# Performance work log

Measured on AMD Instinct MI355X. Metric: run time of the kernel, lower is better.

The kernel has to match this reference:

```python
import jax, jax.numpy as jnp
import numpy as np

B, T, V, D, H, C = 64, 512, 50000, 128, 256, 50


def setup_inputs() -> dict:
    key = jax.random.key(0)
    ks = jax.random.split(key, 15)
    s = 0.05
    rn = lambda k, shape: jax.random.normal(k, shape, jnp.float32) * s
    words = jax.random.randint(ks[0], (B, T), 0, V)
    target = jax.random.randint(ks[1], (B, T), 0, C)
    seq_len = jax.random.randint(ks[2], (B,), T // 2, T + 1)
    seq_len = seq_len.at[0].set(T)  # ensure at least one full-length sequence
    return dict(
        words=words, target=target, seq_len=seq_len,
        emb=rn(ks[3], (V, D)),
        W_ih_f=rn(ks[4], (4 * H, D)), W_hh_f=rn(ks[5], (4 * H, H)), b_f=rn(ks[6], (4 * H,)),
        W_ih_b=rn(ks[7], (4 * H, D)), W_hh_b=rn(ks[8], (4 * H, H)), b_b=rn(ks[9], (4 * H,)),
        fc_W=rn(ks[10], (C, 2 * H)), fc_b=rn(ks[11], (C,)),
        trans=rn(ks[12], (C, C)), start_s=rn(ks[13], (C,)), end_s=rn(ks[14], (C,)),
    )


def _lstm(x, W_ih, W_hh, b):
    # unidirectional LSTM, PyTorch gate order (i, f, g, o). x: [B,T,D] -> h: [B,T,H]
    Hh = W_hh.shape[1]
    xg = jnp.einsum('btd,gd->btg', x, W_ih) + b  # [B,T,4H]

    def step(carry, xt):
        h, c = carry
        g = xt + h @ W_hh.T
        i, f, gg, o = jnp.split(g, 4, axis=-1)
        c = jax.nn.sigmoid(f) * c + jax.nn.sigmoid(i) * jnp.tanh(gg)
        h = jax.nn.sigmoid(o) * jnp.tanh(c)
        return (h, c), h

    h0 = jnp.zeros((x.shape[0], Hh), x.dtype)
    _, hs = jax.lax.scan(step, (h0, h0), jnp.swapaxes(xg, 0, 1))
    return jnp.swapaxes(hs, 0, 1)


def _rev_idx(seq_len, t_len):
    # per-sequence time-reversal indices (packed-sequence semantics for the backward LSTM)
    t = jnp.arange(t_len)[None, :]
    L = seq_len[:, None]
    return jnp.where(t < L, L - 1 - t, t)


def _bilstm_crf_loss(words, target, seq_len, emb, W_ih_f, W_hh_f, b_f,
                     W_ih_b, W_hh_b, b_b, fc_W, fc_b, trans, start_s, end_s):
    x = emb[words]  # [B,T,D]
    h_f = _lstm(x, W_ih_f, W_hh_f, b_f)
    idx = _rev_idx(seq_len, x.shape[1])
    x_rev = jnp.take_along_axis(x, idx[:, :, None], axis=1)
    h_b = jnp.take_along_axis(_lstm(x_rev, W_ih_b, W_hh_b, b_b), idx[:, :, None], axis=1)
    feats = jnp.concatenate([h_f, h_b], axis=-1) @ fc_W.T + fc_b  # [B,T,C]
    logits = jax.nn.log_softmax(feats, axis=-1)
    mask = jnp.arange(x.shape[1])[None, :] < seq_len[:, None]  # [B,T] bool

    # --- CRF normalizer (forward algorithm) ---
    alpha0 = logits[:, 0] + start_s  # [B,C]

    def step(alpha, inp):
        emit_t, m_t = inp  # [B,C], [B]
        tmp = alpha[:, :, None] + trans[None, :, :] + emit_t[:, None, :]
        new = jax.nn.logsumexp(tmp, axis=1)
        return jnp.where(m_t[:, None], new, alpha), None

    alpha, _ = jax.lax.scan(step, alpha0,
                            (jnp.swapaxes(logits, 0, 1)[1:], jnp.swapaxes(mask, 0, 1)[1:]))
    norm = jax.nn.logsumexp(alpha + end_s, axis=1)  # [B]

    # --- gold path score ---
    maskf = mask.astype(logits.dtype)
    emit = jnp.take_along_axis(logits, target[:, :, None], axis=2)[..., 0]  # [B,T]
    trans_sc = trans[target[:, :-1], target[:, 1:]]  # [B,T-1]
    last = target[jnp.arange(target.shape[0]), seq_len - 1]
    gold = (emit * maskf).sum(1) + (trans_sc * maskf[:, 1:]).sum(1) \
           + start_s[target[:, 0]] + end_s[last]

    return jnp.mean(norm - gold)


def reference(words, target, seq_len, emb, W_ih_f, W_hh_f, b_f,
              W_ih_b, W_hh_b, b_b, fc_W, fc_b, trans, start_s, end_s):
    return _bilstm_crf_loss(words, target, seq_len, emb, W_ih_f, W_hh_f, b_f,
                            W_ih_b, W_hh_b, b_b, fc_W, fc_b, trans, start_s, end_s)
```

## Files before the change

kernel.cpp:

```cpp
#include <hip/hip_runtime.h>
#include <hip/hip_bf16.h>

#define BB 64
#define TT 512
#define DD 128
#define HH 256
#define G4 1024
#define CC 50

typedef __bf16 bf16x8 __attribute__((ext_vector_type(8)));
typedef float  f32x4  __attribute__((ext_vector_type(4)));
typedef _Float16 h16x2 __attribute__((ext_vector_type(2)));

#if defined(__has_builtin)
#if __has_builtin(__builtin_amdgcn_fdot2)
#define HAS_FDOT2 1
#endif
#endif

__device__ __forceinline__ float bl16(unsigned u) { return __uint_as_float(u << 16); }
__device__ __forceinline__ float bh16(unsigned u) { return __uint_as_float(u & 0xffff0000u); }

__device__ __forceinline__ float sigf(float x) {
    return 1.f / (1.f + __expf(-x));
}
__device__ __forceinline__ float tanh_s(float x) {
    float ax = fabsf(x);
    float e = __expf(-2.f * ax);
    float r = (1.f - e) / (1.f + e);
    return copysignf(r, x);
}

__device__ __forceinline__ float dot8(float acc, uint4 w, uint4 h) {
#ifdef HAS_FDOT2
    acc = __builtin_amdgcn_fdot2(__builtin_bit_cast(h16x2, w.x),
                                 __builtin_bit_cast(h16x2, h.x), acc, false);
    acc = __builtin_amdgcn_fdot2(__builtin_bit_cast(h16x2, w.y),
                                 __builtin_bit_cast(h16x2, h.y), acc, false);
    acc = __builtin_amdgcn_fdot2(__builtin_bit_cast(h16x2, w.z),
                                 __builtin_bit_cast(h16x2, h.z), acc, false);
    acc = __builtin_amdgcn_fdot2(__builtin_bit_cast(h16x2, w.w),
                                 __builtin_bit_cast(h16x2, h.w), acc, false);
#else
    {
        h16x2 a = __builtin_bit_cast(h16x2, w.x), b = __builtin_bit_cast(h16x2, h.x);
        acc = fmaf((float)a.x, (float)b.x, acc); acc = fmaf((float)a.y, (float)b.y, acc);
        a = __builtin_bit_cast(h16x2, w.y); b = __builtin_bit_cast(h16x2, h.y);
        acc = fmaf((float)a.x, (float)b.x, acc); acc = fmaf((float)a.y, (float)b.y, acc);
        a = __builtin_bit_cast(h16x2, w.z); b = __builtin_bit_cast(h16x2, h.z);
        acc = fmaf((float)a.x, (float)b.x, acc); acc = fmaf((float)a.y, (float)b.y, acc);
        a = __builtin_bit_cast(h16x2, w.w); b = __builtin_bit_cast(h16x2, h.w);
        acc = fmaf((float)a.x, (float)b.x, acc); acc = fmaf((float)a.y, (float)b.y, acc);
    }
#endif
    return acc;
}

__global__ __launch_bounds__(256) void k_cvt(
    const float* __restrict__ src, __hip_bfloat16* __restrict__ dst, int n)
{
    int i = (blockIdx.x * 256 + threadIdx.x) * 8;
    if (i + 8 <= n) {
        float4 a = *(const float4*)(src + i);
        float4 b = *(const float4*)(src + i + 4);
        __hip_bfloat16 o[8];
        o[0] = __float2bfloat16(a.x); o[1] = __float2bfloat16(a.y);
        o[2] = __float2bfloat16(a.z); o[3] = __float2bfloat16(a.w);
        o[4] = __float2bfloat16(b.x); o[5] = __float2bfloat16(b.y);
        o[6] = __float2bfloat16(b.z); o[7] = __float2bfloat16(b.w);
        *(uint4*)(dst + i) = *(const uint4*)o;
    }
}

__global__ __launch_bounds__(256) void k_pack(
    const float* __restrict__ Wf, const float* __restrict__ Wb,
    uint4* __restrict__ Wp)
{
    int blk = blockIdx.x;
    int g   = blk & 3;
    int kc  = (blk >> 2) & 31;
    int dir = blk >> 7;
    int j = threadIdx.x;
    int row = g * 256 + j;
    const float* src = (dir ? Wb : Wf) + (size_t)row * 256 + kc * 8;
    float4 a = *(const float4*)src;
    float4 b = *(const float4*)(src + 4);
    _Float16 o[8];
    o[0] = (_Float16)a.x; o[1] = (_Float16)a.y;
    o[2] = (_Float16)a.z; o[3] = (_Float16)a.w;
    o[4] = (_Float16)b.x; o[5] = (_Float16)b.y;
    o[6] = (_Float16)b.z; o[7] = (_Float16)b.w;
    Wp[((size_t)(dir * 32 + kc) * 4 + g) * 256 + j] = *(const uint4*)o;
}

__global__ __launch_bounds__(256, 2) void k_xg(
    const int* __restrict__ words,
    const float* __restrict__ embf,
    const __hip_bfloat16* __restrict__ Wih,
    const float* __restrict__ bfv, const float* __restrict__ bbv,
    __hip_bfloat16* __restrict__ xg)
{
    __shared__ __align__(16) __hip_bfloat16 A[64][136];
    int tid = threadIdx.x;
    int bt0 = blockIdx.x * 64;

    {
        int r = tid >> 2;
        int c0 = (tid & 3) * 32;
        int word = words[bt0 + r];
        const float* src = embf + (size_t)word * DD + c0;
#pragma unroll
        for (int i = 0; i < 8; ++i) {
            float4 v = *(const float4*)(src + i * 4);
            __hip_bfloat16 o[4] = {__float2bfloat16(v.x), __float2bfloat16(v.y),
                                   __float2bfloat16(v.z), __float2bfloat16(v.w)};
            *(uint2*)&A[r][c0 + i * 4] = *(const uint2*)o;
        }
    }
    __syncthreads();

    int wave = tid >> 6, lane = tid & 63;
    int m = lane & 15, quad = lane >> 4;

    bf16x8 afr[4][4];
#pragma unroll
    for (int ms = 0; ms < 4; ++ms)
#pragma unroll
        for (int kf = 0; kf < 4; ++kf)
            afr[ms][kf] = *(const bf16x8*)&A[ms * 16 + m][quad * 8 + kf * 32];

#pragma unroll 1
    for (int i = 0; i < 32; ++i) {
        int nt = wave * 32 + i;
        int gate_g = nt * 16 + m;
        int dir = gate_g >> 10;
        int gate = gate_g & 1023;
        const __hip_bfloat16* brow = Wih + (size_t)gate_g * DD + quad * 8;
        bf16x8 bfr[4];
#pragma unroll
        for (int kf = 0; kf < 4; ++kf) bfr[kf] = *(const bf16x8*)(brow + kf * 32);
        float bv = dir ? bbv[gate] : bfv[gate];
        size_t dbase = (size_t)dir * (size_t)(BB * TT * G4);

#pragma unroll
        for (int ms = 0; ms < 4; ++ms) {
            f32x4 acc = {0.f, 0.f, 0.f, 0.f};
#pragma unroll
            for (int kf = 0; kf < 4; ++kf)
                acc = __builtin_amdgcn_mfma_f32_16x16x32_bf16(afr[ms][kf], bfr[kf], acc, 0, 0, 0);
#pragma unroll
            for (int r = 0; r < 4; ++r) {
                int btrow = bt0 + ms * 16 + quad * 4 + r;
                xg[dbase + (size_t)btrow * G4 + gate] = __float2bfloat16(acc[r] + bv);
            }
        }
    }
}

__global__ __launch_bounds__(512)
__attribute__((amdgpu_waves_per_eu(2, 2)))
void k_lstm(
    const __hip_bfloat16* __restrict__ xg,
    const uint4* __restrict__ Wp,
    const int* __restrict__ seq_len,
    __hip_bfloat16* __restrict__ hcat)
{
    int b = blockIdx.x & 63;
    int dir = blockIdx.x >> 6;
    int tid = threadIdx.x;
    int j   = tid & 255;
    int half = tid >> 8;

    __shared__ __align__(16) uint4 wlds[12 * 512];
    __shared__ __align__(16) _Float16 hbf[2][HH];
    __shared__ float pbuf[4][HH];

    const uint4* Wd = Wp + (size_t)dir * (32 * 4 * 256);

    uint4 wr[13][4];
#pragma unroll
    for (int kcl = 0; kcl < 13; ++kcl)
#pragma unroll
        for (int g = 0; g < 4; ++g)
            wr[kcl][g] = Wd[(((kcl + 16 * half) * 4 + g) * 256) + j];
#pragma unroll
    for (int kcl = 0; kcl < 13; ++kcl)
#pragma unroll
        for (int g = 0; g < 4; ++g)
            asm volatile("" : "+v"(wr[kcl][g].x), "+v"(wr[kcl][g].y),
                              "+v"(wr[kcl][g].z), "+v"(wr[kcl][g].w));

#pragma unroll
    for (int kcl = 13; kcl < 16; ++kcl)
#pragma unroll
        for (int g = 0; g < 4; ++g)
            wlds[((kcl - 13) * 4 + g) * 512 + tid] =
                Wd[(((kcl + 16 * half) * 4 + g) * 256) + j];

    if (half == 0) hbf[0][j] = (_Float16)0.f;
    float c = 0.f;
    int L = seq_len[b];
    const __hip_bfloat16* xgb = xg + (size_t)dir * (size_t)(BB * TT * G4)
                                   + (size_t)b * TT * G4;

    int tc = dir ? (L - 1) : 0;
    float xv0 = 0.f, xv1 = 0.f, xv2 = 0.f, xv3 = 0.f;
    if (half == 0) {
        const __hip_bfloat16* xr = xgb + (size_t)tc * G4 + j;
        xv0 = __bfloat162float(xr[0]);   xv1 = __bfloat162float(xr[256]);
        xv2 = __bfloat162float(xr[512]); xv3 = __bfloat162float(xr[768]);
    }
    __syncthreads();

    for (int t = 0; t < TT; ++t) {
        int cur = t & 1, nxt = cur ^ 1;
        int tn = t + 1;
        int tcn = dir ? ((tn < L) ? (L - 1 - tn) : tn) : tn;
        bool pf = (tn < TT);
        __hip_bfloat16 p0, p1, p2, p3;
        if (half == 0 && pf) {
            const __hip_bfloat16* xr = xgb + (size_t)tcn * G4 + j;
            p0 = xr[0]; p1 = xr[256]; p2 = xr[512]; p3 = xr[768];
        }

        unsigned off = 0;
        asm volatile("" : "+v"(off));

        const _Float16* hrow = &hbf[cur][half * 128];
        float a0 = 0.f, a1 = 0.f, a2 = 0.f, a3 = 0.f;
#pragma unroll
        for (int kcl = 0; kcl < 13; ++kcl) {
            uint4 hv = *(const uint4*)(hrow + kcl * 8);
            a0 = dot8(a0, wr[kcl][0], hv);
            a1 = dot8(a1, wr[kcl][1], hv);
            a2 = dot8(a2, wr[kcl][2], hv);
            a3 = dot8(a3, wr[kcl][3], hv);
        }
#pragma unroll
        for (int kcl = 13; kcl < 16; ++kcl) {
            uint4 hv = *(const uint4*)(hrow + kcl * 8);
            int m0 = (kcl - 13) * 4;
            a0 = dot8(a0, wlds[(m0 + 0) * 512 + tid + off], hv);
            a1 = dot8(a1, wlds[(m0 + 1) * 512 + tid + off], hv);
            a2 = dot8(a2, wlds[(m0 + 2) * 512 + tid + off], hv);
            a3 = dot8(a3, wlds[(m0 + 3) * 512 + tid + off], hv);
        }

        if (half) {
            pbuf[0][j] = a0; pbuf[1][j] = a1;
            pbuf[2][j] = a2; pbuf[3][j] = a3;
        }
        __syncthreads();

        if (half == 0) {
            float gi = a0 + pbuf[0][j] + xv0;
            float gf = a1 + pbuf[1][j] + xv1;
            float gg = a2 + pbuf[2][j] + xv2;
            float go = a3 + pbuf[3][j] + xv3;
            float i_ = sigf(gi), f_ = sigf(gf), G = tanh_s(gg), o_ = sigf(go);
            c = f_ * c + i_ * G;
            float h = o_ * tanh_s(c);
            hbf[nxt][j] = (_Float16)h;
            hcat[((size_t)(b * TT + tc)) * (2 * HH) + dir * HH + j] = __float2bfloat16(h);
            if (pf) {
                xv0 = __bfloat162float(p0); xv1 = __bfloat162float(p1);
                xv2 = __bfloat162float(p2); xv3 = __bfloat162float(p3);
            }
        }
        tc = tcn;
        __syncthreads();
    }
}

__global__ __launch_bounds__(64) void k_fc(
    const __hip_bfloat16* __restrict__ hcat,
    const __hip_bfloat16* __restrict__ fcW,
    const float* __restrict__ fcb,
    float* __restrict__ logits)
{
    int row = blockIdx.x;
    int tid = threadIdx.x;
    __shared__ __align__(16) float hrow[2 * HH];
    __shared__ float fbuf[CC + 2];

    {
        uint4 v = *(const uint4*)(hcat + (size_t)row * (2 * HH) + tid * 8);
        float* d = &hrow[tid * 8];
        d[0] = bl16(v.x); d[1] = bh16(v.x);
        d[2] = bl16(v.y); d[3] = bh16(v.y);
        d[4] = bl16(v.z); d[5] = bh16(v.z);
        d[6] = bl16(v.w); d[7] = bh16(v.w);
    }
    __syncthreads();

    if (tid < CC) {
        float acc = fcb[tid];
        const uint4* wr = (const uint4*)(fcW + (size_t)tid * (2 * HH));
#pragma unroll 8
        for (int kc = 0; kc < 64; ++kc) {
            uint4 wv = wr[kc];
            float4 h0 = *(const float4*)&hrow[kc * 8];
            float4 h1 = *(const float4*)&hrow[kc * 8 + 4];
            acc = fmaf(bl16(wv.x), h0.x, acc); acc = fmaf(bh16(wv.x), h0.y, acc);
            acc = fmaf(bl16(wv.y), h0.z, acc); acc = fmaf(bh16(wv.y), h0.w, acc);
            acc = fmaf(bl16(wv.z), h1.x, acc); acc = fmaf(bh16(wv.z), h1.y, acc);
            acc = fmaf(bl16(wv.w), h1.z, acc); acc = fmaf(bh16(wv.w), h1.w, acc);
        }
        fbuf[tid] = acc;
    }
    __syncthreads();

    float m = -1e30f;
    for (int i = 0; i < CC; ++i) m = fmaxf(m, fbuf[i]);
    float s = 0.f;
    for (int i = 0; i < CC; ++i) s += __expf(fbuf[i] - m);
    float lns = __logf(s);
    if (tid < CC) logits[(size_t)row * CC + tid] = fbuf[tid] - m - lns;
}

__global__ __launch_bounds__(256) void k_crf(
    const float* __restrict__ logits,
    const int* __restrict__ target,
    const int* __restrict__ seq_len,
    const float* __restrict__ trans,
    const float* __restrict__ start_s,
    const float* __restrict__ end_s,
    float* __restrict__ loss_b)
{
    const float L2E = 1.4426950408889634f;
    const float LN2 = 0.6931471805599453f;
    int b = blockIdx.x;
    int tid = threadIdx.x;
    int q = tid >> 6;
    int j = tid & 63;
    bool act = (j < CC);
    int L = seq_len[b];
    const float* lg = logits + (size_t)b * TT * CC;

    __shared__ float alpha2[64];
    __shared__ float mpart[4][64];
    __shared__ float spart[4][64];
    __shared__ float red[256];
    __shared__ float nbuf[CC + 2];

    int i0 = q * 13;
    int icnt = min(13, CC - i0);
    float treg[13];
    if (act) {
#pragma unroll
        for (int s = 0; s < 13; ++s)
            if (s < icnt) treg[s] = L2E * trans[(i0 + s) * CC + j];
    }
    if (q == 0 && act) alpha2[j] = L2E * (lg[j] + start_s[j]);
    __syncthreads();

    float v[13];
    for (int t = 1; t < L; ++t) {
        float mq = -1e30f;
        if (act) {
#pragma unroll
            for (int s = 0; s < 13; ++s)
                if (s < icnt) { v[s] = alpha2[i0 + s] + treg[s]; mq = fmaxf(mq, v[s]); }
        }
        mpart[q][j] = mq;
        __syncthreads();
        float M = fmaxf(fmaxf(mpart[0][j], mpart[1][j]), fmaxf(mpart[2][j], mpart[3][j]));
        float sq = 0.f;
        if (act) {
#pragma unroll
            for (int s = 0; s < 13; ++s)
                if (s < icnt) sq += exp2f(v[s] - M);
        }
        spart[q][j] = sq;
        __syncthreads();
        if (q == 0 && act) {
            float S = spart[0][j] + spart[1][j] + spart[2][j] + spart[3][j];
            alpha2[j] = M + log2f(S) + L2E * lg[(size_t)t * CC + j];
        }
        __syncthreads();
    }

    if (q == 0 && act) nbuf[j] = alpha2[j] + L2E * end_s[j];

    float gp = 0.f;
    const int* tg = target + b * TT;
    for (int t = tid; t < TT; t += 256) {
        if (t < L) {
            int c = tg[t];
            gp += lg[(size_t)t * CC + c];
            if (t >= 1) gp += trans[tg[t - 1] * CC + c];
        }
    }
    red[tid] = gp;
    __syncthreads();

    if (tid == 0) {
        float m2 = -1e30f;
        for (int i = 0; i < CC; ++i) m2 = fmaxf(m2, nbuf[i]);
        float s2 = 0.f;
        for (int i = 0; i < CC; ++i) s2 += exp2f(nbuf[i] - m2);
        float norm_nat = (m2 + log2f(s2)) * LN2;
        float g = 0.f;
        for (int i = 0; i < 256; ++i) g += red[i];
        g += start_s[tg[0]] + end_s[tg[L - 1]];
        loss_b[b] = norm_nat - g;
    }
}

__global__ void k_fin(const float* __restrict__ loss_b, float* __restrict__ out)
{
    int t = threadIdx.x;
    float v = loss_b[t];
#pragma unroll
    for (int o = 32; o > 0; o >>= 1) v += __shfl_down(v, o);
    if (t == 0) out[0] = v * (1.f / BB);
}

extern "C" void kernel_launch(void* const* d_in, const int* in_sizes, int n_in,
                              void* d_out, int out_size, void* d_ws, size_t ws_size,
                              hipStream_t stream)
{
    const int* words   = (const int*)d_in[0];
    const int* target  = (const int*)d_in[1];
    const int* seq_len = (const int*)d_in[2];
    const float* emb    = (const float*)d_in[3];
    const float* W_ih_f = (const float*)d_in[4];
    const float* W_hh_f = (const float*)d_in[5];
    const float* b_f    = (const float*)d_in[6];
    const float* W_ih_b = (const float*)d_in[7];
    const float* W_hh_b = (const float*)d_in[8];
    const float* b_b    = (const float*)d_in[9];
    const float* fc_W   = (const float*)d_in[10];
    const float* fc_b   = (const float*)d_in[11];
    const float* trans  = (const float*)d_in[12];
    const float* start_s= (const float*)d_in[13];
    const float* end_s  = (const float*)d_in[14];

    char* ws = (char*)d_ws;
    __hip_bfloat16* xg     = (__hip_bfloat16*)ws;
    __hip_bfloat16* hcat   = (__hip_bfloat16*)(ws + 134217728);
    float*          logits = (float*)(ws + 167772160);
    uint4*          Wp     = (uint4*)(ws + 167772160);
    float*          loss_b = (float*)(ws + 174325760);
    __hip_bfloat16* wihall = (__hip_bfloat16*)(ws + 174326016);
    __hip_bfloat16* fcw_bf = (__hip_bfloat16*)(ws + 174850304);

    k_cvt<<<64,  256, 0, stream>>>(W_ih_f, wihall,          131072);
    k_cvt<<<64,  256, 0, stream>>>(W_ih_b, wihall + 131072, 131072);
    k_cvt<<<13,  256, 0, stream>>>(fc_W,   fcw_bf,          25600);
    k_pack<<<256, 256, 0, stream>>>(W_hh_f, W_hh_b, Wp);

    k_xg  <<<512, 256, 0, stream>>>(words, emb, wihall, b_f, b_b, xg);
    k_lstm<<<128, 512, 0, stream>>>(xg, Wp, seq_len, hcat);
    k_fc  <<<32768, 64, 0, stream>>>(hcat, fcw_bf, fc_b, logits);
    k_crf <<<64, 256, 0, stream>>>(logits, target, seq_len, trans, start_s, end_s, loss_b);
    k_fin <<<1, 64, 0, stream>>>(loss_b, (float*)d_out);
}
```

Baseline: 1.809 ms.

## Stream LSTM recurrent weights from cache, batch FC rows, prefetch CRF emissions

The LSTM kernel stops keeping 13 of its 16 weight chunks in registers. It now keeps 4 in registers, 4 in an enlarged LDS buffer, and reloads the other 8 from global memory on every timestep in two staged batches. This frees registers, but adds per-step global or L2 traffic on the serial critical path. The FC kernel now handles four rows per 256-thread block to cut block count, and the CRF kernel prefetches the next timestep's emission value into a register.

```diff
diff --git a/kernel.cpp b/kernel.cpp
--- a/kernel.cpp
+++ b/kernel.cpp
@@ -157,8 +157,7 @@
     }
 }
 
-__global__ __launch_bounds__(512)
-__attribute__((amdgpu_waves_per_eu(2, 2)))
+__global__ __launch_bounds__(512, 2)
 void k_lstm(
     const __hip_bfloat16* __restrict__ xg,
     const uint4* __restrict__ Wp,
@@ -171,31 +170,25 @@
     int j   = tid & 255;
     int half = tid >> 8;
 
-    __shared__ __align__(16) uint4 wlds[12 * 512];
+    __shared__ __align__(16) uint4 wlds[16 * 512];
     __shared__ __align__(16) _Float16 hbf[2][HH];
     __shared__ float pbuf[4][HH];
 
     const uint4* Wd = Wp + (size_t)dir * (32 * 4 * 256);
-
-    uint4 wr[13][4];
-#pragma unroll
-    for (int kcl = 0; kcl < 13; ++kcl)
+    const uint4* Ws = Wd + (size_t)(16 * half) * 4 * 256 + j;
+
+    uint4 wh[4][4];
+#pragma unroll
+    for (int kcl = 0; kcl < 4; ++kcl)
 #pragma unroll
         for (int g = 0; g < 4; ++g)
-            wr[kcl][g] = Wd[(((kcl + 16 * half) * 4 + g) * 256) + j];
-#pragma unroll
-    for (int kcl = 0; kcl < 13; ++kcl)
+            wh[kcl][g] = Ws[(kcl * 4 + g) * 256];
+
+#pragma unroll
+    for (int kcl = 12; kcl < 16; ++kcl)
 #pragma unroll
         for (int g = 0; g < 4; ++g)
-            asm volatile("" : "+v"(wr[kcl][g].x), "+v"(wr[kcl][g].y),
-                              "+v"(wr[kcl][g].z), "+v"(wr[kcl][g].w));
-
-#pragma unroll
-    for (int kcl = 13; kcl < 16; ++kcl)
-#pragma unroll
-        for (int g = 0; g < 4; ++g)
-            wlds[((kcl - 13) * 4 + g) * 512 + tid] =
-                Wd[(((kcl + 16 * half) * 4 + g) * 256) + j];
+            wlds[((kcl - 12) * 4 + g) * 512 + tid] = Ws[(kcl * 4 + g) * 256];
 
     if (half == 0) hbf[0][j] = (_Float16)0.f;
     float c = 0.f;
@@ -212,7 +205,15 @@
     }
     __syncthreads();
 
+#pragma unroll 1
     for (int t = 0; t < TT; ++t) {
+#pragma unroll
+        for (int kcl = 0; kcl < 4; ++kcl)
+#pragma unroll
+            for (int g = 0; g < 4; ++g)
+                asm volatile("" : "+v"(wh[kcl][g].x), "+v"(wh[kcl][g].y),
+                                  "+v"(wh[kcl][g].z), "+v"(wh[kcl][g].w));
+
         int cur = t & 1, nxt = cur ^ 1;
         int tn = t + 1;
         int tcn = dir ? ((tn < L) ? (L - 1 - tn) : tn) : tn;
@@ -228,22 +229,55 @@
 
         const _Float16* hrow = &hbf[cur][half * 128];
         float a0 = 0.f, a1 = 0.f, a2 = 0.f, a3 = 0.f;
-#pragma unroll
-        for (int kcl = 0; kcl < 13; ++kcl) {
+
+        uint4 s1[4][4];
+#pragma unroll
+        for (int q = 0; q < 4; ++q)
+#pragma unroll
+            for (int g = 0; g < 4; ++g)
+                s1[q][g] = Ws[((q + 4) * 4 + g) * 256];
+
+#pragma unroll
+        for (int kcl = 0; kcl < 4; ++kcl) {
             uint4 hv = *(const uint4*)(hrow + kcl * 8);
-            a0 = dot8(a0, wr[kcl][0], hv);
-            a1 = dot8(a1, wr[kcl][1], hv);
-            a2 = dot8(a2, wr[kcl][2], hv);
-            a3 = dot8(a3, wr[kcl][3], hv);
-        }
-#pragma unroll
-        for (int kcl = 13; kcl < 16; ++kcl) {
+            a0 = dot8(a0, wh[kcl][0], hv);
+            a1 = dot8(a1, wh[kcl][1], hv);
+            a2 = dot8(a2, wh[kcl][2], hv);
+            a3 = dot8(a3, wh[kcl][3], hv);
+        }
+
+#pragma unroll
+        for (int kcl = 12; kcl < 16; ++kcl) {
             uint4 hv = *(const uint4*)(hrow + kcl * 8);
-            int m0 = (kcl - 13) * 4;
+            int m0 = (kcl - 12) * 4;
             a0 = dot8(a0, wlds[(m0 + 0) * 512 + tid + off], hv);
             a1 = dot8(a1, wlds[(m0 + 1) * 512 + tid + off], hv);
             a2 = dot8(a2, wlds[(m0 + 2) * 512 + tid + off], hv);
             a3 = dot8(a3, wlds[(m0 + 3) * 512 + tid + off], hv);
+        }
+
+        uint4 s2[4][4];
+#pragma unroll
+        for (int q = 0; q < 4; ++q)
+#pragma unroll
+            for (int g = 0; g < 4; ++g)
+                s2[q][g] = Ws[((q + 8) * 4 + g) * 256];
+
+#pragma unroll
+        for (int q = 0; q < 4; ++q) {
+            uint4 hv = *(const uint4*)(hrow + (q + 4) * 8);
+            a0 = dot8(a0, s1[q][0], hv);
+            a1 = dot8(a1, s1[q][1], hv);
+            a2 = dot8(a2, s1[q][2], hv);
+            a3 = dot8(a3, s1[q][3], hv);
+        }
+#pragma unroll
+        for (int q = 0; q < 4; ++q) {
+            uint4 hv = *(const uint4*)(hrow + (q + 8) * 8);
+            a0 = dot8(a0, s2[q][0], hv);
+            a1 = dot8(a1, s2[q][1], hv);
+            a2 = dot8(a2, s2[q][2], hv);
+            a3 = dot8(a3, s2[q][3], hv);
         }
 
         if (half) {
@@ -272,20 +306,21 @@
     }
 }
 
-__global__ __launch_bounds__(64) void k_fc(
+__global__ __launch_bounds__(256) void k_fc(
     const __hip_bfloat16* __restrict__ hcat,
     const __hip_bfloat16* __restrict__ fcW,
     const float* __restrict__ fcb,
     float* __restrict__ logits)
 {
-    int row = blockIdx.x;
-    int tid = threadIdx.x;
-    __shared__ __align__(16) float hrow[2 * HH];
-    __shared__ float fbuf[CC + 2];
+    int team = threadIdx.x >> 6;
+    int tid  = threadIdx.x & 63;
+    int row  = blockIdx.x * 4 + team;
+    __shared__ __align__(16) float hrow[4][2 * HH];
+    __shared__ float fbuf[4][CC + 2];
 
     {
         uint4 v = *(const uint4*)(hcat + (size_t)row * (2 * HH) + tid * 8);
-        float* d = &hrow[tid * 8];
+        float* d = &hrow[team][tid * 8];
         d[0] = bl16(v.x); d[1] = bh16(v.x);
         d[2] = bl16(v.y); d[3] = bh16(v.y);
         d[4] = bl16(v.z); d[5] = bh16(v.z);
@@ -299,23 +334,23 @@
 #pragma unroll 8
         for (int kc = 0; kc < 64; ++kc) {
             uint4 wv = wr[kc];
-            float4 h0 = *(const float4*)&hrow[kc * 8];
-            float4 h1 = *(const float4*)&hrow[kc * 8 + 4];
+            float4 h0 = *(const float4*)&hrow[team][kc * 8];
+            float4 h1 = *(const float4*)&hrow[team][kc * 8 + 4];
             acc = fmaf(bl16(wv.x), h0.x, acc); acc = fmaf(bh16(wv.x), h0.y, acc);
             acc = fmaf(bl16(wv.y), h0.z, acc); acc = fmaf(bh16(wv.y), h0.w, acc);
             acc = fmaf(bl16(wv.z), h1.x, acc); acc = fmaf(bh16(wv.z), h1.y, acc);
             acc = fmaf(bl16(wv.w), h1.z, acc); acc = fmaf(bh16(wv.w), h1.w, acc);
         }
-        fbuf[tid] = acc;
+        fbuf[team][tid] = acc;
     }
     __syncthreads();
 
     float m = -1e30f;
-    for (int i = 0; i < CC; ++i) m = fmaxf(m, fbuf[i]);
+    for (int i = 0; i < CC; ++i) m = fmaxf(m, fbuf[team][i]);
     float s = 0.f;
-    for (int i = 0; i < CC; ++i) s += __expf(fbuf[i] - m);
+    for (int i = 0; i < CC; ++i) s += __expf(fbuf[team][i] - m);
     float lns = __logf(s);
-    if (tid < CC) logits[(size_t)row * CC + tid] = fbuf[tid] - m - lns;
+    if (tid < CC) logits[(size_t)row * CC + tid] = fbuf[team][tid] - m - lns;
 }
 
 __global__ __launch_bounds__(256) void k_crf(
@@ -355,7 +390,13 @@
     __syncthreads();
 
     float v[13];
+    float lgreg = 0.f;
+    if (q == 0 && act) lgreg = lg[CC + j];
     for (int t = 1; t < L; ++t) {
+        float lgnext = 0.f;
+        if (q == 0 && act && (t + 1) < L)
+            lgnext = lg[(size_t)(t + 1) * CC + j];
+
         float mq = -1e30f;
         if (act) {
 #pragma unroll
@@ -375,8 +416,9 @@
         __syncthreads();
         if (q == 0 && act) {
             float S = spart[0][j] + spart[1][j] + spart[2][j] + spart[3][j];
-            alpha2[j] = M + log2f(S) + L2E * lg[(size_t)t * CC + j];
-        }
+            alpha2[j] = M + log2f(S) + L2E * lgreg;
+        }
+        lgreg = lgnext;
         __syncthreads();
     }
 
@@ -452,7 +494,7 @@
 
     k_xg  <<<512, 256, 0, stream>>>(words, emb, wihall, b_f, b_b, xg);
     k_lstm<<<128, 512, 0, stream>>>(xg, Wp, seq_len, hcat);
-    k_fc  <<<32768, 64, 0, stream>>>(hcat, fcw_bf, fc_b, logits);
+    k_fc  <<<8192, 256, 0, stream>>>(hcat, fcw_bf, fc_b, logits);
     k_crf <<<64, 256, 0, stream>>>(logits, target, seq_len, trans, start_s, end_s, loss_b);
     k_fin <<<1, 64, 0, stream>>>(loss_b, (float*)d_out);
 }
```

Result: slower. 2.081 ms (+15.0%).
